# Kernel tuning notes

Hardware: AMD Instinct MI355X
Metric: run time of the kernel (lower is better)

Reference implementation:

```python
import jax, jax.numpy as jnp
import numpy as np

D = 1024   # d_model
H = 16     # n_heads
S = 2048   # seq_len
HD = D // H  # head_dim = 64
B = 1


def setup_inputs() -> dict:
    key = jax.random.key(0)
    ks = jax.random.split(key, 10)
    s = 0.02
    return {
        "x": jax.random.normal(ks[0], (B, S * D), dtype=jnp.float32),
        "Wq": jax.random.normal(ks[1], (D, D), dtype=jnp.float32) * s,
        "bq": jnp.zeros((D,), dtype=jnp.float32),
        "Wk": jax.random.normal(ks[2], (D, D), dtype=jnp.float32) * s,
        "bk": jnp.zeros((D,), dtype=jnp.float32),
        "Wv": jax.random.normal(ks[3], (D, D), dtype=jnp.float32) * s,
        "bv": jnp.zeros((D,), dtype=jnp.float32),
        "Wo": jax.random.normal(ks[4], (D, D), dtype=jnp.float32) * s,
        "bo": jnp.zeros((D,), dtype=jnp.float32),
        "rel_table": jax.random.normal(ks[5], (2 * S - 1, HD), dtype=jnp.float32),
    }


def reference(x, Wq, bq, Wk, bk, Wv, bv, Wo, bo, rel_table):
    b = x.shape[0]
    x3 = x.reshape(b, S, D)
    # projections; split into heads -> [b, H, S, HD]
    def heads(t):
        return t.reshape(b, S, H, HD).transpose(0, 2, 1, 3)
    Q = heads(x3 @ Wq + bq)
    K = heads(x3 @ Wk + bk)
    V = heads(x3 @ Wv + bv)

    scores = jnp.einsum('bhid,bhjd->bhij', Q, K) / np.sqrt(HD).astype(np.float32)

    # relative position index: clamp(i - j + S - 1, 0, 2S-2)
    pos = jnp.arange(S)
    idx = jnp.clip(pos[:, None] - pos[None, :] + S - 1, 0, 2 * S - 2)  # [S, S]
    # contract Q with the raw table once, then gather per (i, j)
    # (same math as einsum('bhid,ijd->bhij', Q, table[idx]) but avoids [S,S,HD])
    qrel = jnp.einsum('bhid,rd->bhir', Q, rel_table)          # [b, H, S, 2S-1]
    rel_scores = jnp.take_along_axis(qrel, idx[None, None, :, :], axis=-1)  # [b,H,S,S]

    attn = jax.nn.softmax(scores + rel_scores, axis=-1)
    # dropout is identity in eval mode
    out = jnp.einsum('bhij,bhjd->bhid', attn, V)              # [b, H, S, HD]
    out = out.transpose(0, 2, 1, 3).reshape(b, S, D)
    return (out @ Wo + bo).reshape(b, -1)
```

## Files before the change

### kernel.cpp

```cpp
#include <hip/hip_runtime.h>
#include <hip/hip_bf16.h>

#define SEQ 2048
#define DM  1024
#define NH  16
#define HDM 64

typedef __hip_bfloat16 bf16;
typedef __bf16 bhalf8 __attribute__((ext_vector_type(8)));
typedef float floatx4 __attribute__((ext_vector_type(4)));

__device__ __forceinline__ void async_cp16(const void* g, void* l) {
  __builtin_amdgcn_global_load_lds(
      (const __attribute__((address_space(1))) void*)g,
      (__attribute__((address_space(3))) void*)l, 16, 0, 0);
}

__global__ __launch_bounds__(256) void prep(
    const float* __restrict__ x, const float* __restrict__ T,
    const float* __restrict__ W0, const float* __restrict__ W1,
    const float* __restrict__ W2, const float* __restrict__ W3,
    bf16* __restrict__ xbf, bf16* __restrict__ Tbf, bf16* __restrict__ WtBase)
{
  __shared__ float tile[64][69];
  const int b = blockIdx.x;
  const int tid = threadIdx.x;
  if (b < 2048) {
    int c = b * 256 + tid;
    float4 v = *(const float4*)&x[(size_t)c * 4];
    union { bf16 h[4]; float2 f; } u;
    u.h[0] = __float2bfloat16(v.x); u.h[1] = __float2bfloat16(v.y);
    u.h[2] = __float2bfloat16(v.z); u.h[3] = __float2bfloat16(v.w);
    *(float2*)&xbf[(size_t)c * 4] = u.f;
  } else if (b < 2304) {
    int ct = (b - 2048) * 256 + tid;
    union { bf16 h[4]; float2 f; } u;
#pragma unroll
    for (int e = 0; e < 4; ++e) {
      int se = ct * 4 + e;
      if (se >= 4095 * 64) se -= 64;
      u.h[e] = __float2bfloat16(T[se]);
    }
    *(float2*)&Tbf[(size_t)ct * 4] = u.f;
  } else {
    int tb = b - 2304;
    int z = tb >> 8, rem = tb & 255;
    const float* W = (z == 0) ? W0 : (z == 1) ? W1 : (z == 2) ? W2 : W3;
    bf16* Wt = WtBase + (size_t)z * DM * DM;
    const int kb = (rem >> 4) * 64, nb = (rem & 15) * 64;
    const int r = tid >> 4, c4 = (tid & 15) * 4;
#pragma unroll
    for (int rr = 0; rr < 4; ++rr) {
      float4 v = *(const float4*)&W[(size_t)(kb + rr * 16 + r) * DM + nb + c4];
      tile[rr * 16 + r][c4 + 0] = v.x; tile[rr * 16 + r][c4 + 1] = v.y;
      tile[rr * 16 + r][c4 + 2] = v.z; tile[rr * 16 + r][c4 + 3] = v.w;
    }
    __syncthreads();
    const int w = tid >> 6, l = tid & 63;
#pragma unroll
    for (int i = 0; i < 16; ++i) {
      int n = nb + w * 16 + i;
      Wt[(size_t)n * DM + kb + l] = __float2bfloat16(tile[l][w * 16 + i]);
    }
  }
}

__device__ __forceinline__ void gemm64_core(
    const bf16* __restrict__ A, const bf16* __restrict__ Bt,
    bf16* As, bf16* Bs, int bm, int bn, floatx4 (&acc)[4])
{
  const int tid = threadIdx.x;
  const int lane = tid & 63;
  const int w = tid >> 6;
  const int ln15 = lane & 15, quad = lane >> 4;

  for (int k0 = 0; k0 < DM; k0 += 64) {
    {
      int c = w * 64 + lane;
      int row = c >> 2, col = (c & 3) * 8;
      async_cp16(A  + (size_t)(bm + row) * DM + k0 + col,      As + c * 8);
      async_cp16(A  + (size_t)(bm + row) * DM + k0 + 32 + col, As + 2048 + c * 8);
      async_cp16(Bt + (size_t)(bn + row) * DM + k0 + col,      Bs + c * 8);
      async_cp16(Bt + (size_t)(bn + row) * DM + k0 + 32 + col, Bs + 2048 + c * 8);
    }
    __syncthreads();
#pragma unroll
    for (int kk = 0; kk < 2; ++kk) {
      bhalf8 af = *(bhalf8*)&As[kk * 2048 + (w * 16 + ln15) * 32 + quad * 8];
      bhalf8 bfr[4];
#pragma unroll
      for (int j = 0; j < 4; ++j)
        bfr[j] = *(bhalf8*)&Bs[kk * 2048 + (j * 16 + ln15) * 32 + quad * 8];
#pragma unroll
      for (int j = 0; j < 4; ++j)
        acc[j] = __builtin_amdgcn_mfma_f32_16x16x32_bf16(af, bfr[j], acc[j], 0, 0, 0);
    }
    __syncthreads();
  }
}

__global__ __launch_bounds__(256) void gemm_qkv(
    const bf16* __restrict__ A, const bf16* __restrict__ Wt3,
    const float* __restrict__ bq, const float* __restrict__ bk,
    const float* __restrict__ bv, bf16* __restrict__ outbase)
{
  __shared__ __align__(16) bf16 As[64 * 64];
  __shared__ __align__(16) bf16 Bs[64 * 64];
  const int z = blockIdx.z;
  const bf16* Bt = Wt3 + (size_t)z * DM * DM;
  const float* bias = (z == 0) ? bq : (z == 1) ? bk : bv;
  const float kscale = (z == 1) ? 0.125f : 1.0f;
  bf16* C = outbase + (size_t)z * SEQ * DM;
  const int bm = blockIdx.y * 64, bn = blockIdx.x * 64;
  floatx4 acc[4];
#pragma unroll
  for (int j = 0; j < 4; ++j) acc[j] = (floatx4){0.f, 0.f, 0.f, 0.f};
  gemm64_core(A, Bt, As, Bs, bm, bn, acc);

  const int lane = threadIdx.x & 63;
  const int w = threadIdx.x >> 6;
  const int ln15 = lane & 15, quad = lane >> 4;
#pragma unroll
  for (int j = 0; j < 4; ++j) {
    int col = bn + j * 16 + ln15;
    float bv_ = bias[col];
#pragma unroll
    for (int r = 0; r < 4; ++r) {
      int row = bm + w * 16 + quad * 4 + r;
      float v = (acc[j][r] + bv_) * kscale;
      if (z < 2)
        C[((size_t)(col >> 6) * SEQ + row) * HDM + (col & 63)] = __float2bfloat16(v);
      else
        C[(size_t)col * SEQ + row] = __float2bfloat16(v);
    }
  }
}

__global__ __launch_bounds__(256) void gemm_out(
    const bf16* __restrict__ A, const bf16* __restrict__ Bt,
    const float* __restrict__ bias, float* __restrict__ C)
{
  __shared__ __align__(16) bf16 As[64 * 64];
  __shared__ __align__(16) bf16 Bs[64 * 64];
  const int bm = blockIdx.y * 64, bn = blockIdx.x * 64;
  floatx4 acc[4];
#pragma unroll
  for (int j = 0; j < 4; ++j) acc[j] = (floatx4){0.f, 0.f, 0.f, 0.f};
  gemm64_core(A, Bt, As, Bs, bm, bn, acc);

  const int lane = threadIdx.x & 63;
  const int w = threadIdx.x >> 6;
  const int ln15 = lane & 15, quad = lane >> 4;
#pragma unroll
  for (int j = 0; j < 4; ++j) {
    int col = bn + j * 16 + ln15;
    float bv_ = bias[col];
#pragma unroll
    for (int r = 0; r < 4; ++r) {
      int row = bm + w * 16 + quad * 4 + r;
      C[(size_t)row * DM + col] = acc[j][r] + bv_;
    }
  }
}

__global__ __launch_bounds__(256, 2) void attn_flash(
    const bf16* __restrict__ Q, const bf16* __restrict__ K,
    const bf16* __restrict__ Vt, const bf16* __restrict__ Tb,
    bf16* __restrict__ Opart, float* __restrict__ lws)
{
  const int i0   = blockIdx.x * 64;
  const int h    = blockIdx.y;
  const int z    = blockIdx.z;
  const int tid  = threadIdx.x;
  const int lane = tid & 63;
  const int wrow = (tid >> 6) * 16;
  const int ln15 = lane & 15;
  const int quad = lane >> 4;

  __shared__ __align__(16) unsigned char smem[75264];
  bf16*  Ps  = (bf16*)(smem + 49152);
  float* S2c = (float*)(smem + 58368);
  bf16*  Qs  = (bf16*)(smem + 58368);

  const bf16* Qg = Q  + ((size_t)h * SEQ + i0) * HDM;
  const bf16* Kg = K  + (size_t)h * SEQ * HDM;
  const bf16* Vg = Vt + (size_t)h * HDM * SEQ;

  const int r4 = tid >> 2, c8 = (tid & 3) * 8;
  auto stage = [&](int jt_, int b) {
    int j0_ = jt_ * 64;
    int rb_ = i0 - j0_ + SEQ - HDM;
    bf16* Kd = (bf16*)smem + b * 4096;
    bf16* Vd = (bf16*)smem + 8192 + b * 4096;
    bf16* Td = (bf16*)smem + 16384 + b * 4096;
    async_cp16(Kg + (size_t)(j0_ + r4) * HDM + c8,        Kd + tid * 8);
    async_cp16(Kg + (size_t)(j0_ + r4) * HDM + 32 + c8,   Kd + 2048 + tid * 8);
    async_cp16(Vg + (size_t)r4 * SEQ + j0_ + c8,          Vd + tid * 8);
    async_cp16(Vg + (size_t)r4 * SEQ + j0_ + 32 + c8,     Vd + 2048 + tid * 8);
    async_cp16(Tb + (size_t)(rb_ + r4) * HDM + c8,        Td + tid * 8);
    async_cp16(Tb + (size_t)(rb_ + r4) * HDM + 32 + c8,   Td + 2048 + tid * 8);
  };

  const int jt0 = z * 16;
  stage(jt0, 0);

#pragma unroll
  for (int t = 0; t < 2; ++t) {
    int id = tid + t * 256;
    int r = id >> 3, c = (id & 7) * 8;
    *(float4*)&Qs[r * 72 + c] = *(const float4*)&Qg[(size_t)r * HDM + c];
  }
  __syncthreads();

  const bhalf8 aq0 = *(bhalf8*)&Qs[(wrow + ln15) * 72 + quad * 8];
  const bhalf8 aq1 = *(bhalf8*)&Qs[(wrow + ln15) * 72 + quad * 8 + 32];

  floatx4 o[4];
  float lsum[4];
#pragma unroll
  for (int c = 0; c < 4; ++c) { o[c] = (floatx4){0.f, 0.f, 0.f, 0.f}; lsum[c] = 0.f; }

  const int rb0 = i0 - jt0 * 64 + SEQ - HDM;
  floatx4 carry[4];
#pragma unroll
  for (int ct = 0; ct < 4; ++ct) {
    const bf16* tr = Tb + (size_t)(rb0 + 64 + ct * 16 + ln15) * HDM + quad * 8;
    bhalf8 b0 = *(const bhalf8*)tr;
    bhalf8 b1 = *(const bhalf8*)(tr + 32);
    floatx4 a = (floatx4){0.f, 0.f, 0.f, 0.f};
    a = __builtin_amdgcn_mfma_f32_16x16x32_bf16(aq0, b0, a, 0, 0, 0);
    a = __builtin_amdgcn_mfma_f32_16x16x32_bf16(aq1, b1, a, 0, 0, 0);
    carry[ct] = a;
  }

  int cur = 0;
  for (int jt = jt0; jt < jt0 + 16; ++jt) {
    __syncthreads();
    if (jt + 1 < jt0 + 16) stage(jt + 1, cur ^ 1);
    const bf16* Ksc = (bf16*)smem + cur * 4096;
    const bf16* Vsc = (bf16*)smem + 8192 + cur * 4096;
    const bf16* Tsc = (bf16*)smem + 16384 + cur * 4096;

    floatx4 fresh[4];
#pragma unroll
    for (int ct = 0; ct < 4; ++ct) {
      bhalf8 b0 = *(bhalf8*)&Tsc[(ct * 16 + ln15) * 32 + quad * 8];
      bhalf8 b1 = *(bhalf8*)&Tsc[2048 + (ct * 16 + ln15) * 32 + quad * 8];
      floatx4 a = (floatx4){0.f, 0.f, 0.f, 0.f};
      a = __builtin_amdgcn_mfma_f32_16x16x32_bf16(aq0, b0, a, 0, 0, 0);
      a = __builtin_amdgcn_mfma_f32_16x16x32_bf16(aq1, b1, a, 0, 0, 0);
      fresh[ct] = a;
    }
#pragma unroll
    for (int ct = 0; ct < 4; ++ct) {
      int t = ct * 16 + ln15;
#pragma unroll
      for (int r = 0; r < 4; ++r) {
        int row = wrow + quad * 4 + r;
        if (t >= row) S2c[row * 66 + (row + 63 - t)] = fresh[ct][r];
        else          S2c[row * 66 + (row - 1 - t)] = carry[ct][r];
      }
      carry[ct] = fresh[ct];
    }

#pragma unroll
    for (int ct = 0; ct < 4; ++ct) {
      floatx4 s2f;
#pragma unroll
      for (int r = 0; r < 4; ++r)
        s2f[r] = S2c[(wrow + quad * 4 + r) * 66 + ct * 16 + ln15];
      bhalf8 b0 = *(bhalf8*)&Ksc[(ct * 16 + ln15) * 32 + quad * 8];
      bhalf8 b1 = *(bhalf8*)&Ksc[2048 + (ct * 16 + ln15) * 32 + quad * 8];
      floatx4 a = __builtin_amdgcn_mfma_f32_16x16x32_bf16(aq0, b0, s2f, 0, 0, 0);
      a = __builtin_amdgcn_mfma_f32_16x16x32_bf16(aq1, b1, a, 0, 0, 0);
#pragma unroll
      for (int r = 0; r < 4; ++r) {
        float p = __expf(a[r]);
        lsum[r] += p;
        Ps[(wrow + quad * 4 + r) * 72 + ct * 16 + ln15] = __float2bfloat16(p);
      }
    }

    bhalf8 ap0 = *(bhalf8*)&Ps[(wrow + ln15) * 72 + quad * 8];
    bhalf8 ap1 = *(bhalf8*)&Ps[(wrow + ln15) * 72 + quad * 8 + 32];
#pragma unroll
    for (int ct = 0; ct < 4; ++ct) {
      bhalf8 b0 = *(bhalf8*)&Vsc[(ct * 16 + ln15) * 32 + quad * 8];
      bhalf8 b1 = *(bhalf8*)&Vsc[2048 + (ct * 16 + ln15) * 32 + quad * 8];
      o[ct] = __builtin_amdgcn_mfma_f32_16x16x32_bf16(ap0, b0, o[ct], 0, 0, 0);
      o[ct] = __builtin_amdgcn_mfma_f32_16x16x32_bf16(ap1, b1, o[ct], 0, 0, 0);
    }
    cur ^= 1;
  }

  bf16* Oz = Opart + (size_t)z * SEQ * DM;
#pragma unroll
  for (int r = 0; r < 4; ++r) {
    float l = lsum[r];
    l += __shfl_xor(l, 1); l += __shfl_xor(l, 2);
    l += __shfl_xor(l, 4); l += __shfl_xor(l, 8);
    float inv = 1.f / l;
    int row = i0 + wrow + quad * 4 + r;
#pragma unroll
    for (int ct = 0; ct < 4; ++ct)
      Oz[(size_t)row * DM + h * HDM + ct * 16 + ln15] =
          __float2bfloat16(o[ct][r] * inv);
    if (ln15 == 0)
      lws[((size_t)z * NH + h) * SEQ + row] = l;
  }
}

__global__ __launch_bounds__(256) void attn_merge(
    const bf16* __restrict__ O0, const bf16* __restrict__ O1,
    const float* __restrict__ lws, bf16* __restrict__ O)
{
  const int i = blockIdx.x;
  const int tid = threadIdx.x;
  __shared__ float w0s[NH], w1s[NH];
  if (tid < NH) {
    float l0 = lws[((size_t)0 * NH + tid) * SEQ + i];
    float l1 = lws[((size_t)1 * NH + tid) * SEQ + i];
    float inv = 1.f / (l0 + l1);
    w0s[tid] = l0 * inv; w1s[tid] = l1 * inv;
  }
  __syncthreads();
  const int d = tid * 4;
  const float w0 = w0s[d >> 6], w1 = w1s[d >> 6];
  union { bf16 h[4]; float2 f; } a0, a1, ov;
  a0.f = *(const float2*)&O0[(size_t)i * DM + d];
  a1.f = *(const float2*)&O1[(size_t)i * DM + d];
#pragma unroll
  for (int e = 0; e < 4; ++e)
    ov.h[e] = __float2bfloat16(w0 * __bfloat162float(a0.h[e]) +
                               w1 * __bfloat162float(a1.h[e]));
  *(float2*)&O[(size_t)i * DM + d] = ov.f;
}

extern "C" void kernel_launch(void* const* d_in, const int* in_sizes, int n_in,
                              void* d_out, int out_size, void* d_ws, size_t ws_size,
                              hipStream_t stream) {
  const float* x   = (const float*)d_in[0];
  const float* Wq  = (const float*)d_in[1];
  const float* bq  = (const float*)d_in[2];
  const float* Wk  = (const float*)d_in[3];
  const float* bk  = (const float*)d_in[4];
  const float* Wv  = (const float*)d_in[5];
  const float* bv  = (const float*)d_in[6];
  const float* Wo  = (const float*)d_in[7];
  const float* bo  = (const float*)d_in[8];
  const float* rel = (const float*)d_in[9];
  float* out = (float*)d_out;

  const size_t SD = (size_t)SEQ * DM;
  bf16* qws = (bf16*)d_ws;
  bf16* kws = qws + SD;
  bf16* vws = kws + SD;
  bf16* ows = vws + SD;
  bf16* xbf = ows + SD;
  bf16* wt  = xbf + SD;
  bf16* tbf = wt + 4 * (size_t)DM * DM;
  bf16* opart = tbf + (size_t)4096 * HDM;
  float* lws  = (float*)(opart + 2 * SD);

  prep<<<3328, 256, 0, stream>>>(x, rel, Wq, Wk, Wv, Wo, xbf, tbf, wt);
  gemm_qkv<<<dim3(16, 32, 3), 256, 0, stream>>>(xbf, wt, bq, bk, bv, qws);
  attn_flash<<<dim3(SEQ / 64, NH, 2), 256, 0, stream>>>(qws, kws, vws, tbf,
                                                        opart, lws);
  attn_merge<<<SEQ, 256, 0, stream>>>(opart, opart + SD, lws, ows);
  gemm_out<<<dim3(16, 32), 256, 0, stream>>>(ows, wt + 3 * (size_t)DM * DM, bo, out);
}
```

Baseline: 202.8 us.

## Load K/V/T fragments directly from global in attention; swizzle GEMM LDS tiles

```diff
diff --git a/kernel.cpp b/kernel.cpp
--- a/kernel.cpp
+++ b/kernel.cpp
@@ -73,24 +73,23 @@
   const int lane = tid & 63;
   const int w = tid >> 6;
   const int ln15 = lane & 15, quad = lane >> 4;
+  const int qs8  = (quad ^ ((ln15 >> 1) & 3)) * 8;
+  const int srow = tid >> 2;
+  const int scol = ((tid & 3) ^ ((tid >> 3) & 3)) * 8;
 
   for (int k0 = 0; k0 < DM; k0 += 64) {
-    {
-      int c = w * 64 + lane;
-      int row = c >> 2, col = (c & 3) * 8;
-      async_cp16(A  + (size_t)(bm + row) * DM + k0 + col,      As + c * 8);
-      async_cp16(A  + (size_t)(bm + row) * DM + k0 + 32 + col, As + 2048 + c * 8);
-      async_cp16(Bt + (size_t)(bn + row) * DM + k0 + col,      Bs + c * 8);
-      async_cp16(Bt + (size_t)(bn + row) * DM + k0 + 32 + col, Bs + 2048 + c * 8);
-    }
+    async_cp16(A  + (size_t)(bm + srow) * DM + k0 + scol,      As + tid * 8);
+    async_cp16(A  + (size_t)(bm + srow) * DM + k0 + 32 + scol, As + 2048 + tid * 8);
+    async_cp16(Bt + (size_t)(bn + srow) * DM + k0 + scol,      Bs + tid * 8);
+    async_cp16(Bt + (size_t)(bn + srow) * DM + k0 + 32 + scol, Bs + 2048 + tid * 8);
     __syncthreads();
 #pragma unroll
     for (int kk = 0; kk < 2; ++kk) {
-      bhalf8 af = *(bhalf8*)&As[kk * 2048 + (w * 16 + ln15) * 32 + quad * 8];
+      bhalf8 af = *(bhalf8*)&As[kk * 2048 + (w * 16 + ln15) * 32 + qs8];
       bhalf8 bfr[4];
 #pragma unroll
       for (int j = 0; j < 4; ++j)
-        bfr[j] = *(bhalf8*)&Bs[kk * 2048 + (j * 16 + ln15) * 32 + quad * 8];
+        bfr[j] = *(bhalf8*)&Bs[kk * 2048 + (j * 16 + ln15) * 32 + qs8];
 #pragma unroll
       for (int j = 0; j < 4; ++j)
         acc[j] = __builtin_amdgcn_mfma_f32_16x16x32_bf16(af, bfr[j], acc[j], 0, 0, 0);
@@ -177,32 +176,14 @@
   const int ln15 = lane & 15;
   const int quad = lane >> 4;
 
-  __shared__ __align__(16) unsigned char smem[75264];
-  bf16*  Ps  = (bf16*)(smem + 49152);
-  float* S2c = (float*)(smem + 58368);
-  bf16*  Qs  = (bf16*)(smem + 58368);
+  __shared__ __align__(16) unsigned char smem[26112];
+  float* S2c = (float*)smem;
+  bf16*  Ps  = (bf16*)(smem + 16896);
+  bf16*  Qs  = (bf16*)smem;
 
   const bf16* Qg = Q  + ((size_t)h * SEQ + i0) * HDM;
   const bf16* Kg = K  + (size_t)h * SEQ * HDM;
   const bf16* Vg = Vt + (size_t)h * HDM * SEQ;
-
-  const int r4 = tid >> 2, c8 = (tid & 3) * 8;
-  auto stage = [&](int jt_, int b) {
-    int j0_ = jt_ * 64;
-    int rb_ = i0 - j0_ + SEQ - HDM;
-    bf16* Kd = (bf16*)smem + b * 4096;
-    bf16* Vd = (bf16*)smem + 8192 + b * 4096;
-    bf16* Td = (bf16*)smem + 16384 + b * 4096;
-    async_cp16(Kg + (size_t)(j0_ + r4) * HDM + c8,        Kd + tid * 8);
-    async_cp16(Kg + (size_t)(j0_ + r4) * HDM + 32 + c8,   Kd + 2048 + tid * 8);
-    async_cp16(Vg + (size_t)r4 * SEQ + j0_ + c8,          Vd + tid * 8);
-    async_cp16(Vg + (size_t)r4 * SEQ + j0_ + 32 + c8,     Vd + 2048 + tid * 8);
-    async_cp16(Tb + (size_t)(rb_ + r4) * HDM + c8,        Td + tid * 8);
-    async_cp16(Tb + (size_t)(rb_ + r4) * HDM + 32 + c8,   Td + 2048 + tid * 8);
-  };
-
-  const int jt0 = z * 16;
-  stage(jt0, 0);
 
 #pragma unroll
   for (int t = 0; t < 2; ++t) {
@@ -211,15 +192,16 @@
     *(float4*)&Qs[r * 72 + c] = *(const float4*)&Qg[(size_t)r * HDM + c];
   }
   __syncthreads();
-
   const bhalf8 aq0 = *(bhalf8*)&Qs[(wrow + ln15) * 72 + quad * 8];
   const bhalf8 aq1 = *(bhalf8*)&Qs[(wrow + ln15) * 72 + quad * 8 + 32];
+  __syncthreads();
 
   floatx4 o[4];
   float lsum[4];
 #pragma unroll
   for (int c = 0; c < 4; ++c) { o[c] = (floatx4){0.f, 0.f, 0.f, 0.f}; lsum[c] = 0.f; }
 
+  const int jt0 = z * 16;
   const int rb0 = i0 - jt0 * 64 + SEQ - HDM;
   floatx4 carry[4];
 #pragma unroll
@@ -233,19 +215,16 @@
     carry[ct] = a;
   }
 
-  int cur = 0;
   for (int jt = jt0; jt < jt0 + 16; ++jt) {
-    __syncthreads();
-    if (jt + 1 < jt0 + 16) stage(jt + 1, cur ^ 1);
-    const bf16* Ksc = (bf16*)smem + cur * 4096;
-    const bf16* Vsc = (bf16*)smem + 8192 + cur * 4096;
-    const bf16* Tsc = (bf16*)smem + 16384 + cur * 4096;
+    const int j0 = jt * 64;
+    const int rb = i0 - j0 + SEQ - HDM;
 
     floatx4 fresh[4];
 #pragma unroll
     for (int ct = 0; ct < 4; ++ct) {
-      bhalf8 b0 = *(bhalf8*)&Tsc[(ct * 16 + ln15) * 32 + quad * 8];
-      bhalf8 b1 = *(bhalf8*)&Tsc[2048 + (ct * 16 + ln15) * 32 + quad * 8];
+      const bf16* tr = Tb + (size_t)(rb + ct * 16 + ln15) * HDM + quad * 8;
+      bhalf8 b0 = *(const bhalf8*)tr;
+      bhalf8 b1 = *(const bhalf8*)(tr + 32);
       floatx4 a = (floatx4){0.f, 0.f, 0.f, 0.f};
       a = __builtin_amdgcn_mfma_f32_16x16x32_bf16(aq0, b0, a, 0, 0, 0);
       a = __builtin_amdgcn_mfma_f32_16x16x32_bf16(aq1, b1, a, 0, 0, 0);
@@ -269,8 +248,9 @@
 #pragma unroll
       for (int r = 0; r < 4; ++r)
         s2f[r] = S2c[(wrow + quad * 4 + r) * 66 + ct * 16 + ln15];
-      bhalf8 b0 = *(bhalf8*)&Ksc[(ct * 16 + ln15) * 32 + quad * 8];
-      bhalf8 b1 = *(bhalf8*)&Ksc[2048 + (ct * 16 + ln15) * 32 + quad * 8];
+      const bf16* kr = Kg + (size_t)(j0 + ct * 16 + ln15) * HDM + quad * 8;
+      bhalf8 b0 = *(const bhalf8*)kr;
+      bhalf8 b1 = *(const bhalf8*)(kr + 32);
       floatx4 a = __builtin_amdgcn_mfma_f32_16x16x32_bf16(aq0, b0, s2f, 0, 0, 0);
       a = __builtin_amdgcn_mfma_f32_16x16x32_bf16(aq1, b1, a, 0, 0, 0);
 #pragma unroll
@@ -285,12 +265,12 @@
     bhalf8 ap1 = *(bhalf8*)&Ps[(wrow + ln15) * 72 + quad * 8 + 32];
 #pragma unroll
     for (int ct = 0; ct < 4; ++ct) {
-      bhalf8 b0 = *(bhalf8*)&Vsc[(ct * 16 + ln15) * 32 + quad * 8];
-      bhalf8 b1 = *(bhalf8*)&Vsc[2048 + (ct * 16 + ln15) * 32 + quad * 8];
+      const bf16* vr = Vg + (size_t)(ct * 16 + ln15) * SEQ + j0 + quad * 8;
+      bhalf8 b0 = *(const bhalf8*)vr;
+      bhalf8 b1 = *(const bhalf8*)(vr + 32);
       o[ct] = __builtin_amdgcn_mfma_f32_16x16x32_bf16(ap0, b0, o[ct], 0, 0, 0);
       o[ct] = __builtin_amdgcn_mfma_f32_16x16x32_bf16(ap1, b1, o[ct], 0, 0, 0);
     }
-    cur ^= 1;
   }
 
   bf16* Oz = Opart + (size_t)z * SEQ * DM;
```

Result: slower. 322.5 us (+59.0%).

## Use 128x128 tiles for QKV GEMM and XOR-swizzle LDS layouts

Applied to the files above, without the earlier changes.

```diff
diff --git a/kernel.cpp b/kernel.cpp
--- a/kernel.cpp
+++ b/kernel.cpp
@@ -73,24 +73,23 @@
   const int lane = tid & 63;
   const int w = tid >> 6;
   const int ln15 = lane & 15, quad = lane >> 4;
+  const int qs8  = (quad ^ ((ln15 >> 1) & 3)) * 8;
+  const int srow = tid >> 2;
+  const int scol = ((tid & 3) ^ ((tid >> 3) & 3)) * 8;
 
   for (int k0 = 0; k0 < DM; k0 += 64) {
-    {
-      int c = w * 64 + lane;
-      int row = c >> 2, col = (c & 3) * 8;
-      async_cp16(A  + (size_t)(bm + row) * DM + k0 + col,      As + c * 8);
-      async_cp16(A  + (size_t)(bm + row) * DM + k0 + 32 + col, As + 2048 + c * 8);
-      async_cp16(Bt + (size_t)(bn + row) * DM + k0 + col,      Bs + c * 8);
-      async_cp16(Bt + (size_t)(bn + row) * DM + k0 + 32 + col, Bs + 2048 + c * 8);
-    }
+    async_cp16(A  + (size_t)(bm + srow) * DM + k0 + scol,      As + tid * 8);
+    async_cp16(A  + (size_t)(bm + srow) * DM + k0 + 32 + scol, As + 2048 + tid * 8);
+    async_cp16(Bt + (size_t)(bn + srow) * DM + k0 + scol,      Bs + tid * 8);
+    async_cp16(Bt + (size_t)(bn + srow) * DM + k0 + 32 + scol, Bs + 2048 + tid * 8);
     __syncthreads();
 #pragma unroll
     for (int kk = 0; kk < 2; ++kk) {
-      bhalf8 af = *(bhalf8*)&As[kk * 2048 + (w * 16 + ln15) * 32 + quad * 8];
+      bhalf8 af = *(bhalf8*)&As[kk * 2048 + (w * 16 + ln15) * 32 + qs8];
       bhalf8 bfr[4];
 #pragma unroll
       for (int j = 0; j < 4; ++j)
-        bfr[j] = *(bhalf8*)&Bs[kk * 2048 + (j * 16 + ln15) * 32 + quad * 8];
+        bfr[j] = *(bhalf8*)&Bs[kk * 2048 + (j * 16 + ln15) * 32 + qs8];
 #pragma unroll
       for (int j = 0; j < 4; ++j)
         acc[j] = __builtin_amdgcn_mfma_f32_16x16x32_bf16(af, bfr[j], acc[j], 0, 0, 0);
@@ -99,39 +98,75 @@
   }
 }
 
-__global__ __launch_bounds__(256) void gemm_qkv(
+__global__ __launch_bounds__(256) void gemm_qkv128(
     const bf16* __restrict__ A, const bf16* __restrict__ Wt3,
     const float* __restrict__ bq, const float* __restrict__ bk,
     const float* __restrict__ bv, bf16* __restrict__ outbase)
 {
-  __shared__ __align__(16) bf16 As[64 * 64];
-  __shared__ __align__(16) bf16 Bs[64 * 64];
+  __shared__ __align__(16) bf16 As[128 * 64];
+  __shared__ __align__(16) bf16 Bs[128 * 64];
   const int z = blockIdx.z;
   const bf16* Bt = Wt3 + (size_t)z * DM * DM;
   const float* bias = (z == 0) ? bq : (z == 1) ? bk : bv;
   const float kscale = (z == 1) ? 0.125f : 1.0f;
   bf16* C = outbase + (size_t)z * SEQ * DM;
-  const int bm = blockIdx.y * 64, bn = blockIdx.x * 64;
-  floatx4 acc[4];
-#pragma unroll
-  for (int j = 0; j < 4; ++j) acc[j] = (floatx4){0.f, 0.f, 0.f, 0.f};
-  gemm64_core(A, Bt, As, Bs, bm, bn, acc);
-
-  const int lane = threadIdx.x & 63;
-  const int w = threadIdx.x >> 6;
+  const int bm = blockIdx.y * 128, bn = blockIdx.x * 128;
+  const int tid = threadIdx.x;
+  const int lane = tid & 63, w = tid >> 6;
   const int ln15 = lane & 15, quad = lane >> 4;
-#pragma unroll
-  for (int j = 0; j < 4; ++j) {
-    int col = bn + j * 16 + ln15;
+  const int wr = (w >> 1) * 64, wc = (w & 1) * 64;
+
+  floatx4 acc[4][4];
+#pragma unroll
+  for (int mi = 0; mi < 4; ++mi)
+#pragma unroll
+    for (int nj = 0; nj < 4; ++nj) acc[mi][nj] = (floatx4){0.f, 0.f, 0.f, 0.f};
+
+  for (int k0 = 0; k0 < DM; k0 += 64) {
+#pragma unroll
+    for (int t = 0; t < 4; ++t) {
+      int cid = t * 256 + tid;
+      int row = cid >> 3;
+      int scol = ((cid & 7) ^ (row & 7)) * 8;
+      async_cp16(A  + (size_t)(bm + row) * DM + k0 + scol, As + cid * 8);
+      async_cp16(Bt + (size_t)(bn + row) * DM + k0 + scol, Bs + cid * 8);
+    }
+    __syncthreads();
+#pragma unroll
+    for (int kk = 0; kk < 2; ++kk) {
+      const int chs = ((kk * 4 + quad) ^ (ln15 & 7)) * 8;
+      bhalf8 af[4], bfr[4];
+#pragma unroll
+      for (int mi = 0; mi < 4; ++mi)
+        af[mi] = *(bhalf8*)&As[(wr + mi * 16 + ln15) * 64 + chs];
+#pragma unroll
+      for (int nj = 0; nj < 4; ++nj)
+        bfr[nj] = *(bhalf8*)&Bs[(wc + nj * 16 + ln15) * 64 + chs];
+#pragma unroll
+      for (int mi = 0; mi < 4; ++mi)
+#pragma unroll
+        for (int nj = 0; nj < 4; ++nj)
+          acc[mi][nj] = __builtin_amdgcn_mfma_f32_16x16x32_bf16(
+              af[mi], bfr[nj], acc[mi][nj], 0, 0, 0);
+    }
+    __syncthreads();
+  }
+
+#pragma unroll
+  for (int nj = 0; nj < 4; ++nj) {
+    int col = bn + wc + nj * 16 + ln15;
     float bv_ = bias[col];
 #pragma unroll
-    for (int r = 0; r < 4; ++r) {
-      int row = bm + w * 16 + quad * 4 + r;
-      float v = (acc[j][r] + bv_) * kscale;
-      if (z < 2)
-        C[((size_t)(col >> 6) * SEQ + row) * HDM + (col & 63)] = __float2bfloat16(v);
-      else
-        C[(size_t)col * SEQ + row] = __float2bfloat16(v);
+    for (int mi = 0; mi < 4; ++mi) {
+#pragma unroll
+      for (int r = 0; r < 4; ++r) {
+        int row = bm + wr + mi * 16 + quad * 4 + r;
+        float v = (acc[mi][nj][r] + bv_) * kscale;
+        if (z < 2)
+          C[((size_t)(col >> 6) * SEQ + row) * HDM + (col & 63)] = __float2bfloat16(v);
+        else
+          C[(size_t)col * SEQ + row] = __float2bfloat16(v);
+      }
     }
   }
 }
@@ -363,7 +398,7 @@
   float* lws  = (float*)(opart + 2 * SD);
 
   prep<<<3328, 256, 0, stream>>>(x, rel, Wq, Wk, Wv, Wo, xbf, tbf, wt);
-  gemm_qkv<<<dim3(16, 32, 3), 256, 0, stream>>>(xbf, wt, bq, bk, bv, qws);
+  gemm_qkv128<<<dim3(8, 16, 3), 256, 0, stream>>>(xbf, wt, bq, bk, bv, qws);
   attn_flash<<<dim3(SEQ / 64, NH, 2), 256, 0, stream>>>(qws, kws, vws, tbf,
                                                         opart, lws);
   attn_merge<<<SEQ, 256, 0, stream>>>(opart, opart + SD, lws, ows);
```

Result: no change. 203.1 us (+0.1%).
